# Kernel optimization log

Measured on AMD Instinct MI355X. Metric: run time of the kernel, lower is better.

## Reference

```python
import jax, jax.numpy as jnp
import numpy as np

WSCALE = 0.05  # keep qk logits in a stable range for softmax

def setup_inputs() -> dict:
    key = jax.random.key(0)
    ks = jax.random.split(key, 7)
    B, C, H, W = 8, 256, 64, 64
    d = C // 8
    x = jax.random.normal(ks[0], (B, C, H, W), dtype=jnp.float32)
    Wq = jax.random.normal(ks[1], (d, C), dtype=jnp.float32) * WSCALE
    Wk = jax.random.normal(ks[2], (d, C), dtype=jnp.float32) * WSCALE
    Wv = jax.random.normal(ks[3], (C, C), dtype=jnp.float32) * WSCALE
    bq = jnp.zeros((d,), jnp.float32)
    bk = jnp.zeros((d,), jnp.float32)
    bv = jnp.zeros((C,), jnp.float32)
    return {"x": x, "Wq": Wq, "bq": bq, "Wk": Wk, "bk": bk, "Wv": Wv, "bv": bv}

def reference(x, Wq, bq, Wk, bk, Wv, bv):
    B, C, H, W = x.shape
    N = H * W
    xf = x.reshape(B, C, N)                                  # [B,C,N]
    # 1x1 convs == per-pixel linear projections
    q = jnp.einsum('dc,bcn->bdn', Wq, xf) + bq[None, :, None]  # [B,d,N]
    k = jnp.einsum('dc,bcn->bdn', Wk, xf) + bk[None, :, None]  # [B,d,N]
    v = jnp.einsum('ec,bcn->ben', Wv, xf) + bv[None, :, None]  # [B,C,N]
    # attn[b,i,j] = q_i . k_j ; softmax over j (keys)
    attn = jax.nn.softmax(jnp.einsum('bdi,bdj->bij', q, k), axis=-1)  # [B,N,N]
    # out[b,c,i] = sum_j v[b,c,j] * attn[b,i,j]
    out = jnp.einsum('bcj,bij->bci', v, attn)                # [B,C,N]
    return out.reshape(B, C, H, W)
```

## Files before the change

### kernel.cpp

```cpp
#include <hip/hip_runtime.h>
#include <math.h>

#define NB 8
#define NC 256
#define ND 32
#define NN 4096
#define NM 320
#define LOG2E 1.44269504088896f
#define XSTR 264

typedef short short8 __attribute__((ext_vector_type(8)));
typedef float f32x4 __attribute__((ext_vector_type(4)));

__device__ __forceinline__ unsigned int f2bf_u(float f) {
    return (__float_as_uint(f) + 0x8000u) >> 16;
}
__device__ __forceinline__ unsigned short f2bf(float f) {
    return (unsigned short)f2bf_u(f);
}

__global__ __launch_bounds__(256) void repack_kernel(
    const float* __restrict__ Wq, const float* __restrict__ bq,
    const float* __restrict__ Wk, const float* __restrict__ bk,
    const float* __restrict__ Wv, const float* __restrict__ bv,
    unsigned short* __restrict__ wp, float* __restrict__ bias)
{
    const int T    = blockIdx.x * 256 + threadIdx.x;
    const int j    = T & 7;
    const int lane = (T >> 3) & 63;
    const int ks   = (T >> 9) & 7;
    const int mt   = T >> 12;
    const int m = mt * 16 + (lane & 15);
    const int k = ks * 32 + ((lane >> 4) << 3) + j;
    float wv;
    if (m < 32)       wv = Wq[m * NC + k] * LOG2E;
    else if (m < 64)  wv = Wk[(m - 32) * NC + k];
    else              wv = Wv[(m - 64) * NC + k];
    wp[T] = f2bf(wv);
    if (T < NM) {
        float bb;
        if (T < 32)      bb = bq[T] * LOG2E;
        else if (T < 64) bb = bk[T - 32];
        else             bb = bv[T - 64];
        bias[T] = bb;
    }
}

__global__ __launch_bounds__(256, 4) void proj_kernel(
    const float* __restrict__ x,
    const unsigned short* __restrict__ wp,
    const float* __restrict__ bias,
    unsigned short* __restrict__ q_ws,
    unsigned short* __restrict__ k_ws,
    unsigned short* __restrict__ v_ws)
{
    __shared__ __align__(16) unsigned short xs[32 * XSTR];

    const int b  = blockIdx.x >> 7;
    const int n0 = (blockIdx.x & 127) << 5;
    const int t  = threadIdx.x;

    {
        const int n  = t & 31;
        const int cg = t >> 5;
        const float* xb = x + (size_t)b * NC * NN + n0 + n;
        #pragma unroll
        for (int it = 0; it < 8; ++it) {
            const int c = 32 * it + 4 * cg;
            const float x0 = xb[(size_t)(c + 0) * NN];
            const float x1 = xb[(size_t)(c + 1) * NN];
            const float x2 = xb[(size_t)(c + 2) * NN];
            const float x3 = xb[(size_t)(c + 3) * NN];
            uint2 pk;
            pk.x = (f2bf_u(x1) << 16) | f2bf_u(x0);
            pk.y = (f2bf_u(x3) << 16) | f2bf_u(x2);
            *(uint2*)(xs + n * XSTR + c) = pk;
        }
    }
    __syncthreads();

    const int w    = t >> 6;
    const int lane = t & 63;
    const int li = lane & 15;
    const int qd = lane >> 4;

    f32x4 acc[5][2];
    #pragma unroll
    for (int u = 0; u < 5; ++u) {
        const int mt = w + 4 * u;
        const f32x4 b4 = *(const f32x4*)(bias + mt * 16 + qd * 4);
        acc[u][0] = b4; acc[u][1] = b4;
    }

    #pragma unroll
    for (int ks = 0; ks < 8; ++ks) {
        short8 bf[2];
        #pragma unroll
        for (int nf = 0; nf < 2; ++nf)
            bf[nf] = *(const short8*)(xs + (nf * 16 + li) * XSTR + ks * 32 + qd * 8);
        #pragma unroll
        for (int u = 0; u < 5; ++u) {
            const int mt = w + 4 * u;
            const short8 af = *(const short8*)(wp + (size_t)((mt * 8 + ks) * 64 + lane) * 8);
            acc[u][0] = __builtin_amdgcn_mfma_f32_16x16x32_bf16(af, bf[0], acc[u][0], 0, 0, 0);
            acc[u][1] = __builtin_amdgcn_mfma_f32_16x16x32_bf16(af, bf[1], acc[u][1], 0, 0, 0);
        }
    }

    #pragma unroll
    for (int u = 0; u < 5; ++u) {
        const int mt = w + 4 * u;
        if (mt < 4) {
            unsigned short* dst = (mt < 2) ? q_ws : k_ws;
            const int d0 = (mt & 1) * 16 + qd * 4;
            #pragma unroll
            for (int nf = 0; nf < 2; ++nf) {
                const int n = n0 + nf * 16 + li;
                uint2 pk;
                pk.x = (f2bf_u(acc[u][nf][1]) << 16) | f2bf_u(acc[u][nf][0]);
                pk.y = (f2bf_u(acc[u][nf][3]) << 16) | f2bf_u(acc[u][nf][2]);
                *(uint2*)(dst + ((size_t)b * NN + n) * ND + d0) = pk;
            }
        } else {
            const int c0 = (mt - 4) * 16 + qd * 4;
            #pragma unroll
            for (int nf = 0; nf < 2; ++nf) {
                const int n = n0 + nf * 16 + li;
                #pragma unroll
                for (int r = 0; r < 4; ++r)
                    v_ws[((size_t)b * NC + c0 + r) * NN + n] = f2bf(acc[u][nf][r]);
            }
        }
    }
}

__global__ __launch_bounds__(256, 4) void attn_kernel(
    const unsigned short* __restrict__ q_ws,
    const unsigned short* __restrict__ k_ws,
    const unsigned short* __restrict__ v_ws,
    float* __restrict__ out)
{
    __shared__ __align__(16) unsigned short Pb[2][4 * 16 * 64];
    __shared__ float lred[4][16];

    const int b   = blockIdx.x & 7;
    const int idx = blockIdx.x >> 3;
    const int i0  = (idx >> 1) * 64;
    const int ch  = (idx & 1) * 128;
    const int w    = threadIdx.x >> 6;
    const int lane = threadIdx.x & 63;
    const int li = lane & 15;
    const int qd = lane >> 4;
    const int rot = (li & 3) << 2;
    const int c0 = ch + w * 32;

    const int rpos0 = (2 * qd + rot) & 15;
    const int rpos1 = (8 + 2 * qd + rot) & 15;

    const short8 qf = *(const short8*)(q_ws + ((size_t)b * NN + i0 + 16 * w + li) * ND + qd * 8);
    const unsigned short* kb  = k_ws + ((size_t)b * NN + li) * ND + qd * 8;
    const unsigned short* vb0 = v_ws + ((size_t)b * NC + c0 + li) * NN + qd * 8;
    const unsigned short* vb1 = vb0 + (size_t)16 * NN;

    unsigned short* PA = &Pb[0][0];
    unsigned short* PB = &Pb[1][0];

    f32x4 o[4][2];
    #pragma unroll
    for (int sb = 0; sb < 4; ++sb) { o[sb][0] = (f32x4){0,0,0,0}; o[sb][1] = (f32x4){0,0,0,0}; }
    float l_loc = 0.f;
    const f32x4 z4 = {0.f, 0.f, 0.f, 0.f};

    short8 kf[4], vfA[2][2], vfB[2][2];

    auto LKF = [&](int j0) {
        #pragma unroll
        for (int tt = 0; tt < 4; ++tt)
            kf[tt] = *(const short8*)(kb + (size_t)(j0 + 16 * tt) * ND);
    };
    auto LVF = [&](int j0, short8 (&vf)[2][2]) {
        vf[0][0] = *(const short8*)(vb0 + j0);
        vf[0][1] = *(const short8*)(vb0 + j0 + 32);
        vf[1][0] = *(const short8*)(vb1 + j0);
        vf[1][1] = *(const short8*)(vb1 + j0 + 32);
    };
    auto DOS = [&](unsigned short* P) {
        unsigned short* Pw = P + (w * 16 + li) * 64;
        #pragma unroll
        for (int tt = 0; tt < 4; ++tt) {
            const f32x4 s = __builtin_amdgcn_mfma_f32_16x16x32_bf16(kf[tt], qf, z4, 0, 0, 0);
            const float p0 = __builtin_amdgcn_exp2f(s[0]);
            const float p1 = __builtin_amdgcn_exp2f(s[1]);
            const float p2 = __builtin_amdgcn_exp2f(s[2]);
            const float p3 = __builtin_amdgcn_exp2f(s[3]);
            l_loc += (p0 + p1) + (p2 + p3);
            const unsigned u0 = __float_as_uint(p0) + 0x8000u;
            const unsigned u1 = __float_as_uint(p1) + 0x8000u;
            const unsigned u2 = __float_as_uint(p2) + 0x8000u;
            const unsigned u3 = __float_as_uint(p3) + 0x8000u;
            uint2 pk;
            pk.x = __builtin_amdgcn_perm(u1, u0, 0x07060302u);
            pk.y = __builtin_amdgcn_perm(u3, u2, 0x07060302u);
            const int wp = (4 * tt + qd + rot) & 15;
            *(uint2*)(Pw + wp * 4) = pk;
        }
    };
    auto DOPV = [&](const unsigned short* P, const short8 (&vf)[2][2]) {
        #pragma unroll
        for (int sb = 0; sb < 4; ++sb) {
            const unsigned short* Pr = P + (sb * 16 + li) * 64;
            const short8 pf0 = *(const short8*)(Pr + rpos0 * 4);
            const short8 pf1 = *(const short8*)(Pr + rpos1 * 4);
            o[sb][0] = __builtin_amdgcn_mfma_f32_16x16x32_bf16(vf[0][0], pf0, o[sb][0], 0, 0, 0);
            o[sb][0] = __builtin_amdgcn_mfma_f32_16x16x32_bf16(vf[0][1], pf1, o[sb][0], 0, 0, 0);
            o[sb][1] = __builtin_amdgcn_mfma_f32_16x16x32_bf16(vf[1][0], pf0, o[sb][1], 0, 0, 0);
            o[sb][1] = __builtin_amdgcn_mfma_f32_16x16x32_bf16(vf[1][1], pf1, o[sb][1], 0, 0, 0);
        }
    };

    LKF(0); LVF(0, vfA);
    DOS(PA);
    __syncthreads();
    int j0 = 64;
    for (int it = 0; it < 31; ++it) {
        LKF(j0); LVF(j0, vfB);
        DOPV(PA, vfA);
        DOS(PB);
        __syncthreads();
        j0 += 64;
        LKF(j0); LVF(j0, vfA);
        DOPV(PB, vfB);
        DOS(PA);
        __syncthreads();
        j0 += 64;
    }
    LKF(j0); LVF(j0, vfB);
    DOPV(PA, vfA);
    DOS(PB);
    __syncthreads();
    DOPV(PB, vfB);

    l_loc += __shfl_xor(l_loc, 16, 64);
    l_loc += __shfl_xor(l_loc, 32, 64);
    if (lane < 16) lred[w][li] = l_loc;
    __syncthreads();
    float linv[4];
    #pragma unroll
    for (int sb = 0; sb < 4; ++sb)
        linv[sb] = 1.0f / lred[sb][li];

    #pragma unroll
    for (int sb = 0; sb < 4; ++sb)
        #pragma unroll
        for (int ct = 0; ct < 2; ++ct) {
            const int c = c0 + ct * 16 + qd * 4;
            float* op = out + ((size_t)b * NC + c) * NN + i0 + 16 * sb + li;
            #pragma unroll
            for (int r = 0; r < 4; ++r)
                op[(size_t)r * NN] = o[sb][ct][r] * linv[sb];
        }
}

extern "C" void kernel_launch(void* const* d_in, const int* in_sizes, int n_in,
                              void* d_out, int out_size, void* d_ws, size_t ws_size,
                              hipStream_t stream) {
    const float* x  = (const float*)d_in[0];
    const float* Wq = (const float*)d_in[1];
    const float* bq = (const float*)d_in[2];
    const float* Wk = (const float*)d_in[3];
    const float* bk = (const float*)d_in[4];
    const float* Wv = (const float*)d_in[5];
    const float* bv = (const float*)d_in[6];
    float* out = (float*)d_out;

    unsigned short* q_ws = (unsigned short*)d_ws;
    unsigned short* k_ws = q_ws + (size_t)NB * NN * ND;
    unsigned short* v_ws = k_ws + (size_t)NB * NN * ND;
    unsigned short* wp   = v_ws + (size_t)NB * NC * NN;
    float*          bias = (float*)(wp + (size_t)NM * NC);

    repack_kernel<<<NM * NC / 256, 256, 0, stream>>>(Wq, bq, Wk, bk, Wv, bv, wp, bias);
    proj_kernel<<<NB * (NN / 32), 256, 0, stream>>>(x, wp, bias, q_ws, k_ws, v_ws);
    attn_kernel<<<NB * (NN / 64) * 2, 256, 0, stream>>>(q_ws, k_ws, v_ws, out);
}
```

Baseline: 277.1 us.

## Halve attention query tile, split keys across waves, pad P buffer, use LDS-only barrier

The attention kernel now handles 32 queries per block instead of 64, which doubles the grid. The four waves split the score computation into two query subtiles and two key halves, and the two partial row sums are combined at the end. The P scratch buffer gets a 72-element row pitch in place of the rotated-index swizzle. `__syncthreads` becomes an inline barrier that waits only on LDS counters, so global prefetches are not drained at each barrier. The projection kernel swaps the MFMA operand roles, which gives packed V stores but scalar 2-byte Q/K stores. Halving the query tile doubles how often each block re-reads K and V from L2.

```diff
diff --git a/kernel.cpp b/kernel.cpp
--- a/kernel.cpp
+++ b/kernel.cpp
@@ -11,6 +11,8 @@
 
 typedef short short8 __attribute__((ext_vector_type(8)));
 typedef float f32x4 __attribute__((ext_vector_type(4)));
+
+#define LDS_BARRIER() asm volatile("s_waitcnt lgkmcnt(0)\ns_barrier" ::: "memory")
 
 __device__ __forceinline__ unsigned int f2bf_u(float f) {
     return (__float_as_uint(f) + 0x8000u) >> 16;
@@ -87,48 +89,48 @@
     f32x4 acc[5][2];
     #pragma unroll
     for (int u = 0; u < 5; ++u) {
-        const int mt = w + 4 * u;
-        const f32x4 b4 = *(const f32x4*)(bias + mt * 16 + qd * 4);
-        acc[u][0] = b4; acc[u][1] = b4;
+        const float bb = bias[(w + 4 * u) * 16 + li];
+        acc[u][0] = (f32x4){bb, bb, bb, bb};
+        acc[u][1] = (f32x4){bb, bb, bb, bb};
     }
 
     #pragma unroll
     for (int ks = 0; ks < 8; ++ks) {
-        short8 bf[2];
-        #pragma unroll
-        for (int nf = 0; nf < 2; ++nf)
-            bf[nf] = *(const short8*)(xs + (nf * 16 + li) * XSTR + ks * 32 + qd * 8);
+        short8 af[2];
+        #pragma unroll
+        for (int mt = 0; mt < 2; ++mt)
+            af[mt] = *(const short8*)(xs + (mt * 16 + li) * XSTR + ks * 32 + qd * 8);
         #pragma unroll
         for (int u = 0; u < 5; ++u) {
-            const int mt = w + 4 * u;
-            const short8 af = *(const short8*)(wp + (size_t)((mt * 8 + ks) * 64 + lane) * 8);
-            acc[u][0] = __builtin_amdgcn_mfma_f32_16x16x32_bf16(af, bf[0], acc[u][0], 0, 0, 0);
-            acc[u][1] = __builtin_amdgcn_mfma_f32_16x16x32_bf16(af, bf[1], acc[u][1], 0, 0, 0);
+            const int ct = w + 4 * u;
+            const short8 bf = *(const short8*)(wp + (size_t)((ct * 8 + ks) * 64 + lane) * 8);
+            acc[u][0] = __builtin_amdgcn_mfma_f32_16x16x32_bf16(af[0], bf, acc[u][0], 0, 0, 0);
+            acc[u][1] = __builtin_amdgcn_mfma_f32_16x16x32_bf16(af[1], bf, acc[u][1], 0, 0, 0);
         }
     }
 
     #pragma unroll
     for (int u = 0; u < 5; ++u) {
-        const int mt = w + 4 * u;
-        if (mt < 4) {
-            unsigned short* dst = (mt < 2) ? q_ws : k_ws;
-            const int d0 = (mt & 1) * 16 + qd * 4;
+        const int ct = w + 4 * u;
+        if (ct < 4) {
+            unsigned short* dst = (ct < 2) ? q_ws : k_ws;
+            const int d = (ct & 1) * 16 + li;
             #pragma unroll
-            for (int nf = 0; nf < 2; ++nf) {
-                const int n = n0 + nf * 16 + li;
+            for (int mt = 0; mt < 2; ++mt)
+                #pragma unroll
+                for (int r = 0; r < 4; ++r) {
+                    const int n = n0 + mt * 16 + 4 * qd + r;
+                    dst[((size_t)b * NN + n) * ND + d] = f2bf(acc[u][mt][r]);
+                }
+        } else {
+            const int cv = (ct - 4) * 16 + li;
+            #pragma unroll
+            for (int mt = 0; mt < 2; ++mt) {
+                const int n = n0 + mt * 16 + 4 * qd;
                 uint2 pk;
-                pk.x = (f2bf_u(acc[u][nf][1]) << 16) | f2bf_u(acc[u][nf][0]);
-                pk.y = (f2bf_u(acc[u][nf][3]) << 16) | f2bf_u(acc[u][nf][2]);
-                *(uint2*)(dst + ((size_t)b * NN + n) * ND + d0) = pk;
-            }
-        } else {
-            const int c0 = (mt - 4) * 16 + qd * 4;
-            #pragma unroll
-            for (int nf = 0; nf < 2; ++nf) {
-                const int n = n0 + nf * 16 + li;
-                #pragma unroll
-                for (int r = 0; r < 4; ++r)
-                    v_ws[((size_t)b * NC + c0 + r) * NN + n] = f2bf(acc[u][nf][r]);
+                pk.x = (f2bf_u(acc[u][mt][1]) << 16) | f2bf_u(acc[u][mt][0]);
+                pk.y = (f2bf_u(acc[u][mt][3]) << 16) | f2bf_u(acc[u][mt][2]);
+                *(uint2*)(v_ws + ((size_t)b * NC + cv) * NN + n) = pk;
             }
         }
     }
@@ -140,43 +142,40 @@
     const unsigned short* __restrict__ v_ws,
     float* __restrict__ out)
 {
-    __shared__ __align__(16) unsigned short Pb[2][4 * 16 * 64];
+    __shared__ __align__(16) unsigned short Pb[2][2][16 * 72];
     __shared__ float lred[4][16];
 
     const int b   = blockIdx.x & 7;
     const int idx = blockIdx.x >> 3;
-    const int i0  = (idx >> 1) * 64;
+    const int i0  = (idx >> 1) * 32;
     const int ch  = (idx & 1) * 128;
     const int w    = threadIdx.x >> 6;
     const int lane = threadIdx.x & 63;
     const int li = lane & 15;
     const int qd = lane >> 4;
-    const int rot = (li & 3) << 2;
-    const int c0 = ch + w * 32;
-
-    const int rpos0 = (2 * qd + rot) & 15;
-    const int rpos1 = (8 + 2 * qd + rot) & 15;
-
-    const short8 qf = *(const short8*)(q_ws + ((size_t)b * NN + i0 + 16 * w + li) * ND + qd * 8);
-    const unsigned short* kb  = k_ws + ((size_t)b * NN + li) * ND + qd * 8;
+    const int sw = w & 1;
+    const int th = w >> 1;
+    const int c0 = ch + 32 * w;
+
+    const short8 qf = *(const short8*)(q_ws + ((size_t)b * NN + i0 + 16 * sw + li) * ND + qd * 8);
+    const unsigned short* kb  = k_ws + ((size_t)b * NN + 32 * th + li) * ND + qd * 8;
     const unsigned short* vb0 = v_ws + ((size_t)b * NC + c0 + li) * NN + qd * 8;
     const unsigned short* vb1 = vb0 + (size_t)16 * NN;
 
-    unsigned short* PA = &Pb[0][0];
-    unsigned short* PB = &Pb[1][0];
-
-    f32x4 o[4][2];
-    #pragma unroll
-    for (int sb = 0; sb < 4; ++sb) { o[sb][0] = (f32x4){0,0,0,0}; o[sb][1] = (f32x4){0,0,0,0}; }
+    unsigned short* PA = &Pb[0][0][0];
+    unsigned short* PB = &Pb[1][0][0];
+
+    f32x4 o[2][2];
+    o[0][0] = (f32x4){0,0,0,0}; o[0][1] = (f32x4){0,0,0,0};
+    o[1][0] = (f32x4){0,0,0,0}; o[1][1] = (f32x4){0,0,0,0};
     float l_loc = 0.f;
     const f32x4 z4 = {0.f, 0.f, 0.f, 0.f};
 
-    short8 kf[4], vfA[2][2], vfB[2][2];
+    short8 kf[2], vfA[2][2], vfB[2][2];
 
     auto LKF = [&](int j0) {
-        #pragma unroll
-        for (int tt = 0; tt < 4; ++tt)
-            kf[tt] = *(const short8*)(kb + (size_t)(j0 + 16 * tt) * ND);
+        kf[0] = *(const short8*)(kb + (size_t)(j0     ) * ND);
+        kf[1] = *(const short8*)(kb + (size_t)(j0 + 16) * ND);
     };
     auto LVF = [&](int j0, short8 (&vf)[2][2]) {
         vf[0][0] = *(const short8*)(vb0 + j0);
@@ -185,9 +184,9 @@
         vf[1][1] = *(const short8*)(vb1 + j0 + 32);
     };
     auto DOS = [&](unsigned short* P) {
-        unsigned short* Pw = P + (w * 16 + li) * 64;
-        #pragma unroll
-        for (int tt = 0; tt < 4; ++tt) {
+        unsigned short* Pw = P + (size_t)sw * (16 * 72) + li * 72 + 32 * th + 4 * qd;
+        #pragma unroll
+        for (int tt = 0; tt < 2; ++tt) {
             const f32x4 s = __builtin_amdgcn_mfma_f32_16x16x32_bf16(kf[tt], qf, z4, 0, 0, 0);
             const float p0 = __builtin_amdgcn_exp2f(s[0]);
             const float p1 = __builtin_amdgcn_exp2f(s[1]);
@@ -201,63 +200,61 @@
             uint2 pk;
             pk.x = __builtin_amdgcn_perm(u1, u0, 0x07060302u);
             pk.y = __builtin_amdgcn_perm(u3, u2, 0x07060302u);
-            const int wp = (4 * tt + qd + rot) & 15;
-            *(uint2*)(Pw + wp * 4) = pk;
+            *(uint2*)(Pw + 16 * tt) = pk;
         }
     };
     auto DOPV = [&](const unsigned short* P, const short8 (&vf)[2][2]) {
         #pragma unroll
-        for (int sb = 0; sb < 4; ++sb) {
-            const unsigned short* Pr = P + (sb * 16 + li) * 64;
-            const short8 pf0 = *(const short8*)(Pr + rpos0 * 4);
-            const short8 pf1 = *(const short8*)(Pr + rpos1 * 4);
-            o[sb][0] = __builtin_amdgcn_mfma_f32_16x16x32_bf16(vf[0][0], pf0, o[sb][0], 0, 0, 0);
-            o[sb][0] = __builtin_amdgcn_mfma_f32_16x16x32_bf16(vf[0][1], pf1, o[sb][0], 0, 0, 0);
-            o[sb][1] = __builtin_amdgcn_mfma_f32_16x16x32_bf16(vf[1][0], pf0, o[sb][1], 0, 0, 0);
-            o[sb][1] = __builtin_amdgcn_mfma_f32_16x16x32_bf16(vf[1][1], pf1, o[sb][1], 0, 0, 0);
+        for (int s = 0; s < 2; ++s) {
+            const unsigned short* Pr = P + (size_t)s * (16 * 72) + li * 72 + qd * 8;
+            const short8 pf0 = *(const short8*)(Pr);
+            const short8 pf1 = *(const short8*)(Pr + 32);
+            o[s][0] = __builtin_amdgcn_mfma_f32_16x16x32_bf16(vf[0][0], pf0, o[s][0], 0, 0, 0);
+            o[s][0] = __builtin_amdgcn_mfma_f32_16x16x32_bf16(vf[0][1], pf1, o[s][0], 0, 0, 0);
+            o[s][1] = __builtin_amdgcn_mfma_f32_16x16x32_bf16(vf[1][0], pf0, o[s][1], 0, 0, 0);
+            o[s][1] = __builtin_amdgcn_mfma_f32_16x16x32_bf16(vf[1][1], pf1, o[s][1], 0, 0, 0);
         }
     };
 
     LKF(0); LVF(0, vfA);
     DOS(PA);
-    __syncthreads();
+    LDS_BARRIER();
     int j0 = 64;
     for (int it = 0; it < 31; ++it) {
         LKF(j0); LVF(j0, vfB);
         DOPV(PA, vfA);
         DOS(PB);
-        __syncthreads();
+        LDS_BARRIER();
         j0 += 64;
         LKF(j0); LVF(j0, vfA);
         DOPV(PB, vfB);
         DOS(PA);
-        __syncthreads();
+        LDS_BARRIER();
         j0 += 64;
     }
     LKF(j0); LVF(j0, vfB);
     DOPV(PA, vfA);
     DOS(PB);
-    __syncthreads();
+    LDS_BARRIER();
     DOPV(PB, vfB);
 
     l_loc += __shfl_xor(l_loc, 16, 64);
     l_loc += __shfl_xor(l_loc, 32, 64);
     if (lane < 16) lred[w][li] = l_loc;
     __syncthreads();
-    float linv[4];
-    #pragma unroll
-    for (int sb = 0; sb < 4; ++sb)
-        linv[sb] = 1.0f / lred[sb][li];
-
-    #pragma unroll
-    for (int sb = 0; sb < 4; ++sb)
-        #pragma unroll
-        for (int ct = 0; ct < 2; ++ct) {
-            const int c = c0 + ct * 16 + qd * 4;
-            float* op = out + ((size_t)b * NC + c) * NN + i0 + 16 * sb + li;
+    float linv[2];
+    linv[0] = 1.0f / (lred[0][li] + lred[2][li]);
+    linv[1] = 1.0f / (lred[1][li] + lred[3][li]);
+
+    #pragma unroll
+    for (int s = 0; s < 2; ++s)
+        #pragma unroll
+        for (int mt = 0; mt < 2; ++mt) {
+            const int c = c0 + mt * 16 + qd * 4;
+            float* op = out + ((size_t)b * NC + c) * NN + i0 + 16 * s + li;
             #pragma unroll
             for (int r = 0; r < 4; ++r)
-                op[(size_t)r * NN] = o[sb][ct][r] * linv[sb];
+                op[(size_t)r * NN] = o[s][mt][r] * linv[s];
         }
 }
 
@@ -281,5 +278,5 @@
 
     repack_kernel<<<NM * NC / 256, 256, 0, stream>>>(Wq, bq, Wk, bk, Wv, bv, wp, bias);
     proj_kernel<<<NB * (NN / 32), 256, 0, stream>>>(x, wp, bias, q_ws, k_ws, v_ws);
-    attn_kernel<<<NB * (NN / 64) * 2, 256, 0, stream>>>(q_ws, k_ws, v_ws, out);
-}
+    attn_kernel<<<NB * (NN / 32) * 2, 256, 0, stream>>>(q_ws, k_ws, v_ws, out);
+}
```

Result: slower. 384.9 us (+38.9%).
